# Optimization experiments

Hardware: AMD Instinct MI355X
Metric: run time of the kernel (lower is better)

## Reference

```python
import jax, jax.numpy as jnp
import numpy as np

B, S, D, H = 2, 2048, 1024, 16
DK = D // H


def setup_inputs() -> dict:
    key = jax.random.key(0)
    ks = jax.random.split(key, 12)
    q = jax.random.normal(ks[0], (B, S, D), dtype=jnp.float32)
    k = jax.random.normal(ks[1], (B, S, D), dtype=jnp.float32)
    v = jax.random.normal(ks[2], (B, S, D), dtype=jnp.float32)
    # causal mask: 1 = attend, 0 = masked (masked_fill(mask==0, -inf))
    mask = jnp.tril(jnp.ones((S, S), dtype=jnp.int32))[None, None]
    w = 0.02
    Wq = jax.random.normal(ks[3], (D, D), dtype=jnp.float32) * w
    bq = jnp.zeros((D,), dtype=jnp.float32)
    Wk = jax.random.normal(ks[4], (D, D), dtype=jnp.float32) * w
    bk = jnp.zeros((D,), dtype=jnp.float32)
    Wv = jax.random.normal(ks[5], (D, D), dtype=jnp.float32) * w
    bv = jnp.zeros((D,), dtype=jnp.float32)
    Wo = jax.random.normal(ks[6], (D, D), dtype=jnp.float32) * w
    bo = jnp.zeros((D,), dtype=jnp.float32)
    return {"q": q, "k": k, "v": v, "mask": mask,
            "Wq": Wq, "bq": bq, "Wk": Wk, "bk": bk,
            "Wv": Wv, "bv": bv, "Wo": Wo, "bo": bo}


def _split_heads(x):
    b, s, _ = x.shape
    return x.reshape(b, s, H, DK).transpose(0, 2, 1, 3)  # [B,H,S,DK]


def reference(q, k, v, mask, Wq, bq, Wk, bk, Wv, bv, Wo, bo):
    qh = _split_heads(q @ Wq.T + bq)
    kh = _split_heads(k @ Wk.T + bk)
    vh = _split_heads(v @ Wv.T + bv)
    scale = 1.0 / jnp.sqrt(jnp.float32(DK))
    scores = jnp.einsum("bhqd,bhkd->bhqk", qh, kh) * scale  # [B,H,S,S]
    scores = jnp.where(mask == 0, -jnp.inf, scores)
    pesos = jax.nn.softmax(scores, axis=-1)
    pesos = jnp.nan_to_num(pesos, nan=0.0)  # fully-masked rows -> 0
    out = jnp.einsum("bhqk,bhkd->bhqd", pesos, vh)
    out = out.transpose(0, 2, 1, 3).reshape(q.shape[0], q.shape[1], D)
    # dropout is identity at inference
    return out @ Wo.T + bo
```

## Files before the change

kernel.cpp:

```cpp
#include <hip/hip_runtime.h>
#include <hip/hip_bf16.h>

#define B_  2
#define S_  2048
#define D_  1024
#define H_  16
#define DK_ 64

using bf16 = __hip_bfloat16;
typedef __bf16 bf16x8 __attribute__((ext_vector_type(8)));
typedef float  f32x4  __attribute__((ext_vector_type(4)));
typedef float  f32x16 __attribute__((ext_vector_type(16)));

__device__ inline void st1(float* p, float v) { *p = v; }
__device__ inline void st1(bf16*  p, float v) { *p = __float2bfloat16(v); }

__device__ inline void gll16(const bf16* g, bf16* l) {
    __builtin_amdgcn_global_load_lds(
        (const __attribute__((address_space(1))) unsigned int*)g,
        (__attribute__((address_space(3))) unsigned int*)l, 16, 0, 0);
}

__device__ inline f32x16 mfma32(bf16x8 a, bf16x8 b, f32x16 c) {
    return __builtin_amdgcn_mfma_f32_32x32x16_bf16(a, b, c, 0, 0, 0);
}

__device__ inline unsigned cvtpk(float lo, float hi) {
    unsigned r;
    asm("v_cvt_pk_bf16_f32 %0, %1, %2" : "=v"(r) : "v"(lo), "v"(hi));
    return r;
}

__device__ inline void plswap(unsigned &d, unsigned &s) {
    asm volatile("v_permlane32_swap_b32 %0, %1" : "+v"(d), "+v"(s));
}

__global__ __launch_bounds__(256) void cvt_kernel(
    const float* __restrict__ s0, const float* __restrict__ s1,
    const float* __restrict__ s2, const float* __restrict__ s3,
    const float* __restrict__ s4, const float* __restrict__ s5,
    const float* __restrict__ s6,
    bf16* __restrict__ d0, bf16* __restrict__ d1, bf16* __restrict__ d2,
    bf16* __restrict__ d3, bf16* __restrict__ d4, bf16* __restrict__ d5,
    bf16* __restrict__ d6, int nbig, int nsmall)
{
    const int z = blockIdx.y;
    const float* s; bf16* d; int n;
    switch (z) {
        case 0: s = s0; d = d0; n = nbig;   break;
        case 1: s = s1; d = d1; n = nbig;   break;
        case 2: s = s2; d = d2; n = nbig;   break;
        case 3: s = s3; d = d3; n = nsmall; break;
        case 4: s = s4; d = d4; n = nsmall; break;
        case 5: s = s5; d = d5; n = nsmall; break;
        default: s = s6; d = d6; n = nsmall; break;
    }
    const int idx = (blockIdx.x * 256 + threadIdx.x) * 4;
    if (idx < n) {
        const float4 v = *reinterpret_cast<const float4*>(s + idx);
        union { ushort4 u; __bf16 h[4]; } r;
        r.h[0] = (__bf16)v.x; r.h[1] = (__bf16)v.y;
        r.h[2] = (__bf16)v.z; r.h[3] = (__bf16)v.w;
        *reinterpret_cast<ushort4*>(d + idx) = r.u;
    }
}

template <typename TC, bool VT3, int BM>
__global__ __launch_bounds__(256, BM == 128 ? 3 : 4) void gemm_bt_kernel(
    const bf16* __restrict__ A0, const bf16* __restrict__ A1, const bf16* __restrict__ A2,
    const bf16* __restrict__ W0, const bf16* __restrict__ W1, const bf16* __restrict__ W2,
    const float* __restrict__ b0, const float* __restrict__ b1, const float* __restrict__ b2,
    TC* __restrict__ C0, TC* __restrict__ C1, TC* __restrict__ C2,
    int M, int N, int K)
{
    const int bid  = blockIdx.x;
    const int ny   = M / BM;
    const int tile = (bid & 7) * (gridDim.x >> 3) + (bid >> 3);
    const int x    = tile & 7;
    const int pair = tile >> 3;
    const int y    = pair % ny;
    const int z    = pair / ny;

    const bf16*  A    = (z == 0) ? A0 : (z == 1) ? A1 : A2;
    const bf16*  W    = (z == 0) ? W0 : (z == 1) ? W1 : W2;
    const float* bias = (z == 0) ? b0 : (z == 1) ? b1 : b2;
    TC*          C    = (z == 0) ? C0 : (z == 1) ? C1 : C2;

    __shared__ bf16 As[BM][32];
    __shared__ bf16 Bs[128][32];

    const int t    = threadIdx.x;
    const int lane = t & 63;
    const int wave = t >> 6;
    const int quad = lane >> 4;
    const int l16  = lane & 15;
    const int wm   = wave >> 1;
    const int wn   = wave & 1;

    const int m0 = y * BM;
    const int n0 = x * 128;

    constexpr int RPW = BM / 4;
    constexpr int MI  = BM / 32;
    const int ar0 = wave * RPW + (lane >> 2);
    const int br0 = wave * 32  + (lane >> 2);
    const int c0  = (lane & 3) * 8;
    const bf16* Ab = A + (size_t)(m0 + ar0) * K + c0;
    const bf16* Bb = W + (size_t)(n0 + br0) * K + c0;
    bf16* asd = &As[wave * RPW][0];
    bf16* bsd = &Bs[wave * 32][0];

    f32x4 acc[MI][4] = {};

    for (int kt = 0; kt < K; kt += 32) {
        __syncthreads();
        gll16(Ab + kt, asd);
        if constexpr (BM == 128) gll16(Ab + 16 * K + kt, asd + 16 * 32);
        gll16(Bb + kt, bsd);
        gll16(Bb + 16 * K + kt, bsd + 16 * 32);
        __syncthreads();

        bf16x8 af[MI], bfr[4];
#pragma unroll
        for (int mi = 0; mi < MI; mi++)
            af[mi] = *reinterpret_cast<const bf16x8*>(&As[wm * (BM / 2) + mi * 16 + l16][quad * 8]);
#pragma unroll
        for (int ni = 0; ni < 4; ni++)
            bfr[ni] = *reinterpret_cast<const bf16x8*>(&Bs[wn * 64 + ni * 16 + l16][quad * 8]);
#pragma unroll
        for (int mi = 0; mi < MI; mi++)
#pragma unroll
            for (int ni = 0; ni < 4; ni++)
                acc[mi][ni] = __builtin_amdgcn_mfma_f32_16x16x32_bf16(
                    af[mi], bfr[ni], acc[mi][ni], 0, 0, 0);
    }

    if (VT3 && z == 2) {
#pragma unroll
        for (int ni = 0; ni < 4; ni++) {
            const int col = n0 + wn * 64 + ni * 16 + l16;
            const float bvv = bias[col];
            const int hh = col >> 6, dh = col & 63;
#pragma unroll
            for (int mi = 0; mi < MI; mi++) {
                const int rb  = m0 + wm * (BM / 2) + mi * 16 + quad * 4;
                const int bb  = rb >> 11;
                const int tok = rb & (S_ - 1);
                union { ushort4 u; __bf16 h[4]; } pk;
#pragma unroll
                for (int i = 0; i < 4; i++)
                    pk.h[i] = (__bf16)(acc[mi][ni][i] + bvv);
                bf16* vt = (bf16*)C + ((size_t)(bb * H_ + hh) * DK_ + dh) * S_ + tok;
                *reinterpret_cast<ushort4*>(vt) = pk.u;
            }
        }
    } else {
#pragma unroll
        for (int ni = 0; ni < 4; ni++) {
            const int col = n0 + wn * 64 + ni * 16 + l16;
            const float bvv = bias[col];
#pragma unroll
            for (int mi = 0; mi < MI; mi++) {
#pragma unroll
                for (int i = 0; i < 4; i++) {
                    const int row = m0 + wm * (BM / 2) + mi * 16 + quad * 4 + i;
                    st1(&C[(size_t)row * N + col], acc[mi][ni][i] + bvv);
                }
            }
        }
    }
}

__global__ __launch_bounds__(256, 2) void attn_kernel(
    const bf16* __restrict__ Qp, const bf16* __restrict__ Kp,
    const bf16* __restrict__ VT, bf16* __restrict__ AO)
{
    const int t    = threadIdx.x;
    const int lane = t & 63;
    const int wave = t >> 6;
    const int r31  = lane & 31;
    const int hl   = lane >> 5;
    const int l7   = lane & 7;

    const int bid = blockIdx.x;
    int til, hb;
    if (bid < 256) { til = 15 - (bid >> 5); hb = bid & 31; }
    else           { til = (bid - 256) >> 5; hb = (bid - 256) & 31; }
    const int h = hb & 15;
    const int b = hb >> 4;
    const size_t bh = (size_t)b * S_ * D_ + (size_t)h * DK_;
    const bf16* vtb = VT + (size_t)(b * H_ + h) * DK_ * S_;

    __shared__ bf16 Ks[4][64][64];
    __shared__ bf16 Vs[4][64][64];

    const int sR  = lane >> 3;
    const int scg = ((lane & 7) ^ sR) * 8;

    const float QSC = 0.18033688f;
    const float NEG = -1e30f;

    bf16x8 ONES;
#pragma unroll
    for (int j = 0; j < 8; j++) ONES[j] = (__bf16)1.0f;

    const int ntot = 2 * til + 2;

    bf16x8 qf[4];
    {
        const bf16* qr = Qp + bh + (size_t)(til * 128 + wave * 32 + r31) * D_ + 8 * hl;
#pragma unroll
        for (int d = 0; d < 4; d++) {
            qf[d] = *reinterpret_cast<const bf16x8*>(qr + 16 * d);
#pragma unroll
            for (int j = 0; j < 8; j++) qf[d][j] = (__bf16)((float)qf[d][j] * QSC);
        }
    }

    f32x16 oacc0 = {}, oacc1 = {}, lacc = {};

    auto stage = [&](int slot) {
        const int k0n = slot * 64;
        const int bb  = slot & 3;
#pragma unroll
        for (int j = 0; j < 2; j++) {
            const int rb = wave * 16 + j * 8;
            gll16(Kp + bh + (size_t)(k0n + rb + sR) * D_ + scg, &Ks[bb][rb][0]);
            gll16(vtb + (size_t)(rb + sR) * S_ + k0n + scg,     &Vs[bb][rb][0]);
        }
    };

    stage(0);
    stage(1);

    for (int it = 0; it < ntot; it++) {
        if (it + 2 < ntot) {
            stage(it + 2);
            asm volatile("s_waitcnt vmcnt(8)" ::: "memory");
        } else if (it + 1 < ntot) {
            asm volatile("s_waitcnt vmcnt(4)" ::: "memory");
        } else {
            asm volatile("s_waitcnt vmcnt(0)" ::: "memory");
        }
        __builtin_amdgcn_s_barrier();

        const int k0  = it * 64;
        const int buf = it & 3;
        const int qw0 = til * 128 + wave * 32;

        if (k0 <= qw0 + 31) {
            f32x16 s0 = {}, s1 = {};
#pragma unroll
            for (int d = 0; d < 4; d++) {
                const int g = ((2 * d + hl) ^ l7) * 8;
                const bf16x8 kf0 = *reinterpret_cast<const bf16x8*>(&Ks[buf][r31][g]);
                const bf16x8 kf1 = *reinterpret_cast<const bf16x8*>(&Ks[buf][32 + r31][g]);
                s0 = mfma32(kf0, qf[d], s0);
                s1 = mfma32(kf1, qf[d], s1);
            }

            if (k0 + 63 > qw0) {
                const int qg = qw0 + r31;
                const int kb = k0 + 4 * hl;
#pragma unroll
                for (int r = 0; r < 16; r++) {
                    const int ko = (r & 3) + 8 * (r >> 2);
                    s0[r] = (kb + ko      <= qg) ? s0[r] : NEG;
                    s1[r] = (kb + 32 + ko <= qg) ? s1[r] : NEG;
                }
            }

#pragma unroll
            for (int r = 0; r < 16; r++) {
                s0[r] = __builtin_amdgcn_exp2f(s0[r]);
                s1[r] = __builtin_amdgcn_exp2f(s1[r]);
            }

            bf16x8 pa[4];
#pragma unroll
            for (int G = 0; G < 2; G++) {
#pragma unroll
                for (int tt = 0; tt < 2; tt++) {
                    unsigned a01, a23, a45, a67;
                    if (G == 0) {
                        a01 = cvtpk(s0[8*tt+0], s0[8*tt+1]);
                        a23 = cvtpk(s0[8*tt+2], s0[8*tt+3]);
                        a45 = cvtpk(s0[8*tt+4], s0[8*tt+5]);
                        a67 = cvtpk(s0[8*tt+6], s0[8*tt+7]);
                    } else {
                        a01 = cvtpk(s1[8*tt+0], s1[8*tt+1]);
                        a23 = cvtpk(s1[8*tt+2], s1[8*tt+3]);
                        a45 = cvtpk(s1[8*tt+4], s1[8*tt+5]);
                        a67 = cvtpk(s1[8*tt+6], s1[8*tt+7]);
                    }
                    plswap(a01, a45);
                    plswap(a23, a67);
                    union { unsigned u[4]; bf16x8 v; } pu;
                    pu.u[0] = a01; pu.u[1] = a23; pu.u[2] = a45; pu.u[3] = a67;
                    pa[2 * G + tt] = pu.v;
                }
            }

#pragma unroll
            for (int s = 0; s < 4; s++) {
                const int g = ((2 * s + hl) ^ l7) * 8;
                const bf16x8 vf0 = *reinterpret_cast<const bf16x8*>(&Vs[buf][r31][g]);
                const bf16x8 vf1 = *reinterpret_cast<const bf16x8*>(&Vs[buf][32 + r31][g]);
                oacc0 = mfma32(pa[s], vf0, oacc0);
                oacc1 = mfma32(pa[s], vf1, oacc1);
                lacc  = mfma32(pa[s], ONES, lacc);
            }
        }
    }

    {
        const int qb0 = til * 128 + wave * 32;
#pragma unroll
        for (int r = 0; r < 16; r++) {
            const int q = qb0 + (r & 3) + 8 * (r >> 2) + 4 * hl;
            const float inv = 1.0f / lacc[r];
            AO[bh + (size_t)q * D_ + r31]      = __float2bfloat16(oacc0[r] * inv);
            AO[bh + (size_t)q * D_ + 32 + r31] = __float2bfloat16(oacc1[r] * inv);
        }
    }
}

extern "C" void kernel_launch(void* const* d_in, const int* in_sizes, int n_in,
                              void* d_out, int out_size, void* d_ws, size_t ws_size,
                              hipStream_t stream)
{
    const float* q  = (const float*)d_in[0];
    const float* k  = (const float*)d_in[1];
    const float* v  = (const float*)d_in[2];
    const float* Wq = (const float*)d_in[4];
    const float* bq = (const float*)d_in[5];
    const float* Wk = (const float*)d_in[6];
    const float* bk = (const float*)d_in[7];
    const float* Wv = (const float*)d_in[8];
    const float* bv = (const float*)d_in[9];
    const float* Wo = (const float*)d_in[10];
    const float* bo = (const float*)d_in[11];
    float* out = (float*)d_out;

    bf16* ws = (bf16*)d_ws;
    const size_t MD = (size_t)(B_ * S_) * D_;
    const size_t WN = (size_t)D_ * D_;
    bf16* qb  = ws;
    bf16* kb  = ws + MD;
    bf16* vb  = ws + 2 * MD;
    bf16* wqb = ws + 3 * MD;
    bf16* wkb = wqb + WN;
    bf16* wvb = wkb + WN;
    bf16* wob = wvb + WN;
    bf16* Qp  = wob + WN;
    bf16* Kp  = Qp + MD;
    bf16* VT  = Kp + MD;
    bf16* AO  = Qp;

    const int M = B_ * S_;

    cvt_kernel<<<dim3((int)(MD / 4 / 256), 7), 256, 0, stream>>>(
        q, k, v, Wq, Wk, Wv, Wo, qb, kb, vb, wqb, wkb, wvb, wob,
        (int)MD, (int)WN);

    gemm_bt_kernel<bf16, true, 128><<<dim3(768), 256, 0, stream>>>(
        qb, kb, vb, wqb, wkb, wvb, bq, bk, bv, Qp, Kp, VT, M, D_, D_);

    attn_kernel<<<dim3(512), 256, 0, stream>>>(Qp, Kp, VT, AO);

    gemm_bt_kernel<float, false, 64><<<dim3(512), 256, 0, stream>>>(
        AO, AO, AO, wob, wob, wob, bo, bo, bo, out, out, out, M, D_, D_);
}
```

Baseline: 218.5 us.

## Restructure attention K/V pipeline to double-buffered 128-key stages

The attention loop now stages 128 keys (two 64-key halves) per iteration into a two-slot double buffer instead of 64 keys into a four-slot ring with prefetch depth two. The wait and barrier move to the end of each iteration with a full vmcnt(0) drain, which halves the number of barriers per block. The cost is a shallower prefetch: each stage's loads must complete within one iteration of compute rather than two, so more load latency may be exposed. Shared memory usage is unchanged.

```diff
diff --git a/kernel.cpp b/kernel.cpp
--- a/kernel.cpp
+++ b/kernel.cpp
@@ -191,8 +191,8 @@
     const size_t bh = (size_t)b * S_ * D_ + (size_t)h * DK_;
     const bf16* vtb = VT + (size_t)(b * H_ + h) * DK_ * S_;
 
-    __shared__ bf16 Ks[4][64][64];
-    __shared__ bf16 Vs[4][64][64];
+    __shared__ bf16 Ks[2][2][64][64];
+    __shared__ bf16 Vs[2][2][64][64];
 
     const int sR  = lane >> 3;
     const int scg = ((lane & 7) ^ sR) * 8;
@@ -204,7 +204,7 @@
 #pragma unroll
     for (int j = 0; j < 8; j++) ONES[j] = (__bf16)1.0f;
 
-    const int ntot = 2 * til + 2;
+    const int ntot = til + 1;
 
     bf16x8 qf[4];
     {
@@ -220,41 +220,41 @@
     f32x16 oacc0 = {}, oacc1 = {}, lacc = {};
 
     auto stage = [&](int slot) {
-        const int k0n = slot * 64;
-        const int bb  = slot & 3;
-#pragma unroll
-        for (int j = 0; j < 2; j++) {
-            const int rb = wave * 16 + j * 8;
-            gll16(Kp + bh + (size_t)(k0n + rb + sR) * D_ + scg, &Ks[bb][rb][0]);
-            gll16(vtb + (size_t)(rb + sR) * S_ + k0n + scg,     &Vs[bb][rb][0]);
+        const int k0n = slot * 128;
+        const int bb  = slot & 1;
+#pragma unroll
+        for (int half = 0; half < 2; half++) {
+            const int kh = k0n + 64 * half;
+#pragma unroll
+            for (int j = 0; j < 2; j++) {
+                const int rb = wave * 16 + j * 8;
+                gll16(Kp + bh + (size_t)(kh + rb + sR) * D_ + scg, &Ks[bb][half][rb][0]);
+                gll16(vtb + (size_t)(rb + sR) * S_ + kh + scg,     &Vs[bb][half][rb][0]);
+            }
         }
     };
 
     stage(0);
-    stage(1);
+    asm volatile("s_waitcnt vmcnt(0)" ::: "memory");
+    __builtin_amdgcn_s_barrier();
 
     for (int it = 0; it < ntot; it++) {
-        if (it + 2 < ntot) {
-            stage(it + 2);
-            asm volatile("s_waitcnt vmcnt(8)" ::: "memory");
-        } else if (it + 1 < ntot) {
-            asm volatile("s_waitcnt vmcnt(4)" ::: "memory");
-        } else {
-            asm volatile("s_waitcnt vmcnt(0)" ::: "memory");
-        }
-        __builtin_amdgcn_s_barrier();
-
-        const int k0  = it * 64;
-        const int buf = it & 3;
+        if (it + 1 < ntot) stage(it + 1);
+
+        const int buf = it & 1;
         const int qw0 = til * 128 + wave * 32;
 
-        if (k0 <= qw0 + 31) {
+#pragma unroll
+        for (int hh = 0; hh < 2; hh++) {
+            const int k0 = it * 128 + 64 * hh;
+            if (k0 > qw0 + 31) continue;
+
             f32x16 s0 = {}, s1 = {};
 #pragma unroll
             for (int d = 0; d < 4; d++) {
                 const int g = ((2 * d + hl) ^ l7) * 8;
-                const bf16x8 kf0 = *reinterpret_cast<const bf16x8*>(&Ks[buf][r31][g]);
-                const bf16x8 kf1 = *reinterpret_cast<const bf16x8*>(&Ks[buf][32 + r31][g]);
+                const bf16x8 kf0 = *reinterpret_cast<const bf16x8*>(&Ks[buf][hh][r31][g]);
+                const bf16x8 kf1 = *reinterpret_cast<const bf16x8*>(&Ks[buf][hh][32 + r31][g]);
                 s0 = mfma32(kf0, qf[d], s0);
                 s1 = mfma32(kf1, qf[d], s1);
             }
@@ -304,13 +304,16 @@
 #pragma unroll
             for (int s = 0; s < 4; s++) {
                 const int g = ((2 * s + hl) ^ l7) * 8;
-                const bf16x8 vf0 = *reinterpret_cast<const bf16x8*>(&Vs[buf][r31][g]);
-                const bf16x8 vf1 = *reinterpret_cast<const bf16x8*>(&Vs[buf][32 + r31][g]);
+                const bf16x8 vf0 = *reinterpret_cast<const bf16x8*>(&Vs[buf][hh][r31][g]);
+                const bf16x8 vf1 = *reinterpret_cast<const bf16x8*>(&Vs[buf][hh][32 + r31][g]);
                 oacc0 = mfma32(pa[s], vf0, oacc0);
                 oacc1 = mfma32(pa[s], vf1, oacc1);
                 lacc  = mfma32(pa[s], ONES, lacc);
             }
         }
+
+        asm volatile("s_waitcnt vmcnt(0)" ::: "memory");
+        __builtin_amdgcn_s_barrier();
     }
 
     {
```

Measured after the change: 216.9 us. About the same (-0.7%).
